# Kernel optimization log

Measured on AMD Instinct MI355X. Metric: run time of the kernel, lower is better.

Reference implementation:

```python
import jax, jax.numpy as jnp
import numpy as np

EPS = 1e-8
N_ITER = 3
S = 8      # n_slots
D = 64     # slot_size
HID = 128  # mlp hidden


def _ln(x, w, b):
    m = jnp.mean(x, axis=-1, keepdims=True)
    v = jnp.var(x, axis=-1, keepdims=True)
    return (x - m) * jax.lax.rsqrt(v + 1e-5) * w + b


def setup_inputs() -> dict:
    key = jax.random.key(0)
    ks = jax.random.split(key, 20)
    B, N, Din = 128, 4096, 64
    g = lambda k, sh, s: (jax.random.normal(k, sh, jnp.float32) * s)
    return {
        "inputs": jax.random.normal(ks[0], (B, N, Din), jnp.float32),
        "eps_noise": jax.random.normal(ks[1], (B, S, D), jnp.float32),
        "slot_mu": g(ks[2], (1, 1, D), 0.1),
        "slot_logvar": g(ks[3], (1, 1, D), 0.1),
        "k_w": g(ks[4], (D, Din), 1.0 / np.sqrt(Din)),
        "v_w": g(ks[5], (D, Din), 1.0 / np.sqrt(Din)),
        "q_w": g(ks[6], (D, D), 1.0 / np.sqrt(D)),
        "ni_w": jnp.ones((Din,), jnp.float32), "ni_b": jnp.zeros((Din,), jnp.float32),
        "ns_w": jnp.ones((D,), jnp.float32),  "ns_b": jnp.zeros((D,), jnp.float32),
        "nr_w": jnp.ones((D,), jnp.float32),  "nr_b": jnp.zeros((D,), jnp.float32),
        "gru_wih": g(ks[7], (3 * D, D), 1.0 / np.sqrt(D)),
        "gru_whh": g(ks[8], (3 * D, D), 1.0 / np.sqrt(D)),
        "gru_bih": jnp.zeros((3 * D,), jnp.float32),
        "gru_bhh": jnp.zeros((3 * D,), jnp.float32),
        "mlp_w1": g(ks[9], (HID, D), 1.0 / np.sqrt(D)),
        "mlp_w2": g(ks[10], (D, HID), 1.0 / np.sqrt(HID)),
        "mlp_b2": jnp.zeros((D,), jnp.float32),
    }


def _gru(x, h, wih, whh, bih, bhh):
    gi = x @ wih.T + bih  # [BS, 3D]
    gh = h @ whh.T + bhh
    i_r, i_z, i_n = jnp.split(gi, 3, axis=-1)
    h_r, h_z, h_n = jnp.split(gh, 3, axis=-1)
    r = jax.nn.sigmoid(i_r + h_r)
    z = jax.nn.sigmoid(i_z + h_z)
    n = jnp.tanh(i_n + r * h_n)
    return (1.0 - z) * n + z * h


def _step(slots, k, v, q_w, ns_w, ns_b, nr_w, nr_b,
          gru_wih, gru_whh, gru_bih, gru_bhh, mlp_w1, mlp_w2, mlp_b2):
    B = slots.shape[0]
    q = _ln(slots, ns_w, ns_b) @ q_w.T                     # [B,S,D]
    logits = jnp.einsum('bnd,bsd->bns', k, q)              # [B,N,S]
    w = jax.nn.softmax(logits, axis=-1) + EPS              # softmax over slots
    w = w / jnp.sum(w, axis=-2, keepdims=True)             # renorm over tokens
    atten_maps = jnp.einsum('bns,bnd->bsd', w, v)          # [B,S,D]
    h = _gru(atten_maps.reshape(B * S, D), slots.reshape(B * S, D),
             gru_wih, gru_whh, gru_bih, gru_bhh)
    h = h + (jax.nn.relu(_ln(h, nr_w, nr_b) @ mlp_w1.T) @ mlp_w2.T + mlp_b2)
    return h.reshape(B, S, D), w


def reference(inputs, eps_noise, slot_mu, slot_logvar, k_w, v_w, q_w,
              ni_w, ni_b, ns_w, ns_b, nr_w, nr_b,
              gru_wih, gru_whh, gru_bih, gru_bhh, mlp_w1, mlp_w2, mlp_b2):
    std = jnp.exp(0.5 * slot_logvar)
    slots = slot_mu + std * eps_noise                      # [B,S,D]
    x = _ln(inputs, ni_w, ni_b)
    k = (x @ k_w.T) / np.sqrt(D).astype(np.float32)        # [B,N,D]
    v = x @ v_w.T
    args = (q_w, ns_w, ns_b, nr_w, nr_b, gru_wih, gru_whh,
            gru_bih, gru_bhh, mlp_w1, mlp_w2, mlp_b2)
    for _ in range(N_ITER):
        slots, w = _step(slots, k, v, *args)
    slots, w = _step(jax.lax.stop_gradient(slots), k, v, *args)
    return slots, w
```

## Files before the change

kernel.cpp:

```cpp
#include <hip/hip_runtime.h>
#include <hip/hip_bf16.h>

#define BB 128
#define NN 4096
#define DD 64
#define SS 8
#define HH 128

typedef __attribute__((ext_vector_type(8))) short short8;
typedef __attribute__((ext_vector_type(4))) short short4v;
typedef __attribute__((ext_vector_type(4))) float f32x4;

__device__ __forceinline__ float warp_red_sum(float v) {
    #pragma unroll
    for (int off = 32; off; off >>= 1) v += __shfl_xor(v, off);
    return v;
}

__device__ __forceinline__ float bcastlane(float v, int l) {
    return __int_as_float(__builtin_amdgcn_readlane(__float_as_int(v), l));
}

__device__ __forceinline__ unsigned short bfu(float f) {
    __hip_bfloat16 h = __float2bfloat16(f);
    return *(unsigned short*)&h;
}

__device__ __forceinline__ unsigned pk2(float a, float b) {
    return (unsigned)bfu(a) | ((unsigned)bfu(b) << 16);
}

__device__ __forceinline__ short4v ds_tr16(unsigned off) {
    short4v r;
    asm volatile("ds_read_b64_tr_b16 %0, %1" : "=v"(r) : "v"(off));
    return r;
}

__global__ __launch_bounds__(256) void prep_kernel(
    const float* __restrict__ v_w, const float* __restrict__ q_w,
    const float* __restrict__ wih, const float* __restrict__ whh,
    const float* __restrict__ w1, const float* __restrict__ w2,
    float* __restrict__ vwT, float* __restrict__ qwT,
    float* __restrict__ wihT, float* __restrict__ whhT,
    float* __restrict__ w1T, float* __restrict__ w2T)
{
    int i0 = blockIdx.x * blockDim.x + threadIdx.x;
    int nthr = gridDim.x * blockDim.x;
    for (int t = i0; t < 4096; t += nthr) {
        int i = t >> 6, o = t & 63;
        vwT[t] = v_w[o * 64 + i];
        qwT[t] = q_w[o * 64 + i];
    }
    for (int t = i0; t < 12288; t += nthr) {
        int r = t / 192, c = t % 192;
        wihT[t] = wih[c * 64 + r];
        whhT[t] = whh[c * 64 + r];
    }
    for (int t = i0; t < 8192; t += nthr) {
        int r = t >> 7, c = t & 127;
        w1T[t] = w1[c * 64 + r];
    }
    for (int t = i0; t < 8192; t += nthr) {
        int r = t >> 6, c = t & 63;
        w2T[t] = w2[c * 128 + r];
    }
}

__global__ __launch_bounds__(256) void init_q_kernel(
    const float* __restrict__ eps, const float* __restrict__ mu,
    const float* __restrict__ lv, const float* __restrict__ qwT,
    const float* __restrict__ k_w,
    const float* __restrict__ nsw, const float* __restrict__ nsb,
    float* __restrict__ slots, unsigned short* __restrict__ qb,
    float* __restrict__ zbuf)
{
    const int tid = threadIdx.x, lane = tid & 63;
    const int row = blockIdx.x * 4 + (tid >> 6);
    const int idx = row * 64 + lane;
    float s0 = mu[lane] + __expf(0.5f * lv[lane]) * eps[idx];
    slots[idx] = s0;
    float m = warp_red_sum(s0) * (1.0f / 64.0f);
    float dx = s0 - m;
    float var = warp_red_sum(dx * dx) * (1.0f / 64.0f);
    float xln = dx * rsqrtf(var + 1e-5f) * nsw[lane] + nsb[lane];
    float q = 0.f;
    #pragma unroll 8
    for (int i = 0; i < 64; ++i) q = fmaf(bcastlane(xln, i), qwT[i * 64 + lane], q);
    float qp = 0.f;
    #pragma unroll 8
    for (int o = 0; o < 64; ++o) qp = fmaf(bcastlane(q, o), k_w[o * 64 + lane], qp);
    qb[idx] = bfu(qp * 0.125f);
    int g = blockIdx.x * 256 + tid;
    for (int j = g; j < 66560; j += 65536) zbuf[j] = 0.f;
}

__global__ __launch_bounds__(256) void phase_a_ln(
    const float* __restrict__ inp, const float* __restrict__ niw, const float* __restrict__ nib,
    unsigned short* __restrict__ xb)
{
    const int tid = threadIdx.x, lane = tid & 63, widx = tid >> 6;
    const int t8 = lane >> 3, d8 = lane & 7;
    const float4 wn0 = *(const float4*)&niw[d8 * 8];
    const float4 wn1 = *(const float4*)&niw[d8 * 8 + 4];
    const float4 bn0 = *(const float4*)&nib[d8 * 8];
    const float4 bn1 = *(const float4*)&nib[d8 * 8 + 4];
    const int tok0 = blockIdx.x * 128;
    #pragma unroll
    for (int it = 0; it < 4; ++it) {
        const int m = widx * 32 + it * 8 + t8;
        const float* rowp = inp + (size_t)(tok0 + m) * 64 + d8 * 8;
        float4 a = *(const float4*)rowp;
        float4 c = *(const float4*)(rowp + 4);
        float s1 = (a.x + a.y + a.z + a.w) + (c.x + c.y + c.z + c.w);
        float s2 = fmaf(a.x, a.x, fmaf(a.y, a.y, fmaf(a.z, a.z, a.w * a.w)));
        s2 = fmaf(c.x, c.x, fmaf(c.y, c.y, fmaf(c.z, c.z, fmaf(c.w, c.w, s2))));
        #pragma unroll
        for (int o = 1; o < 8; o <<= 1) { s1 += __shfl_xor(s1, o); s2 += __shfl_xor(s2, o); }
        float mean = s1 * (1.0f / 64.0f);
        float var = s2 * (1.0f / 64.0f) - mean * mean;
        float rstd = rsqrtf(var + 1e-5f);
        float y[8];
        y[0] = (a.x - mean) * rstd * wn0.x + bn0.x;
        y[1] = (a.y - mean) * rstd * wn0.y + bn0.y;
        y[2] = (a.z - mean) * rstd * wn0.z + bn0.z;
        y[3] = (a.w - mean) * rstd * wn0.w + bn0.w;
        y[4] = (c.x - mean) * rstd * wn1.x + bn1.x;
        y[5] = (c.y - mean) * rstd * wn1.y + bn1.y;
        y[6] = (c.z - mean) * rstd * wn1.z + bn1.z;
        y[7] = (c.w - mean) * rstd * wn1.w + bn1.w;
        uint4 o4;
        o4.x = pk2(y[0], y[1]); o4.y = pk2(y[2], y[3]);
        o4.z = pk2(y[4], y[5]); o4.w = pk2(y[6], y[7]);
        *(uint4*)&xb[(size_t)(tok0 + m) * 64 + d8 * 8] = o4;
    }
}

__global__ __launch_bounds__(256) void attn_mfma(
    const __hip_bfloat16* __restrict__ xb,
    const unsigned short* __restrict__ qb,
    float* __restrict__ numer, float* __restrict__ denom, float* __restrict__ wout)
{
    __shared__ unsigned short smem[11904];
    unsigned short* Qs = smem;
    const int tid = threadIdx.x, lane = tid & 63, widx = tid >> 6;
    unsigned short* wls = smem + 1152 + widx * 640;
    unsigned short* Xw  = smem + 3712 + widx * 2048;
    const int b = blockIdx.y;
    const int quad = lane >> 4, l16 = lane & 15;
    const int twave0 = blockIdx.x * 512 + widx * 128;

    short8 bkA[2][2], bkB[2][2];
    #pragma unroll
    for (int t4h = 0; t4h < 2; ++t4h) {
        const size_t xrow = ((size_t)b * NN + twave0 + t4h * 16 + l16) * 64;
        bkA[t4h][0] = *(const short8*)&xb[xrow + quad * 8];
        bkA[t4h][1] = *(const short8*)&xb[xrow + 32 + quad * 8];
    }

    for (int t = tid; t < 1024; t += 256) {
        int s = t >> 6, dd = t & 63;
        Qs[s * 72 + dd] = (s < 8) ? qb[b * 512 + t] : (unsigned short)0;
    }
    for (int t = lane; t < 320; t += 64) wls[320 + t] = 0;
    __syncthreads();

    short8 aq0 = *(const short8*)&Qs[l16 * 72 + quad * 8];
    short8 aq1 = *(const short8*)&Qs[l16 * 72 + 32 + quad * 8];

    f32x4 accv[4];
    #pragma unroll
    for (int nt = 0; nt < 4; ++nt) accv[nt] = (f32x4){0.f, 0.f, 0.f, 0.f};
    float dacc[4] = {0.f, 0.f, 0.f, 0.f};

    unsigned short* xw0 = Xw + (quad >> 1) * 512 + l16 * 16 + (quad & 1) * 8;
    const unsigned xtr = (unsigned)(size_t)Xw
                       + (unsigned)((quad * 8 + (l16 >> 2)) * 32 + (l16 & 3) * 8);

    auto PROC = [&](short8 (&cur)[2][2], short8 (&nxt)[2][2], int hg, bool pf) {
        const int t0g = twave0 + hg * 32;
        if (pf) {
            #pragma unroll
            for (int t4h = 0; t4h < 2; ++t4h) {
                const size_t xrow = ((size_t)b * NN + t0g + 32 + t4h * 16 + l16) * 64;
                nxt[t4h][0] = *(const short8*)&xb[xrow + quad * 8];
                nxt[t4h][1] = *(const short8*)&xb[xrow + 32 + quad * 8];
            }
        }
        #pragma unroll
        for (int t4h = 0; t4h < 2; ++t4h) {
            const int tok = t0g + t4h * 16 + l16;
            short8 bk0 = cur[t4h][0];
            short8 bk1 = cur[t4h][1];
            *(short8*)(xw0 + t4h * 256) = bk0;
            *(short8*)(xw0 + t4h * 256 + 1024) = bk1;
            f32x4 lg = (f32x4){0.f, 0.f, 0.f, 0.f};
            lg = __builtin_amdgcn_mfma_f32_16x16x32_bf16(aq0, bk0, lg, 0, 0, 0);
            lg = __builtin_amdgcn_mfma_f32_16x16x32_bf16(aq1, bk1, lg, 0, 0, 0);
            float e[4];
            #pragma unroll
            for (int r = 0; r < 4; ++r) e[r] = __expf(lg[r]);
            float s4 = (e[0] + e[1]) + (e[2] + e[3]);
            float stot = s4 + __shfl_xor(s4, 16);
            float rs = __builtin_amdgcn_rcpf(stot);
            float wv[4];
            #pragma unroll
            for (int r = 0; r < 4; ++r) { wv[r] = fmaf(e[r], rs, 1e-8f); dacc[r] += wv[r]; }
            if (quad < 2) {
                #pragma unroll
                for (int r = 0; r < 4; ++r)
                    wls[(quad * 4 + r) * 40 + t4h * 16 + l16] = bfu(wv[r]);
                if (wout)
                    *(float4*)&wout[((size_t)b * NN + tok) * 8 + quad * 4] =
                        make_float4(wv[0], wv[1], wv[2], wv[3]);
            }
        }
        asm volatile("" ::: "memory");
        short8 aw = *(const short8*)&wls[l16 * 40 + quad * 8];
        short4v rlo[4], rhi[4];
        #pragma unroll
        for (int nt = 0; nt < 4; ++nt) {
            rlo[nt] = ds_tr16(xtr + nt * 1024);
            rhi[nt] = ds_tr16(xtr + nt * 1024 + 128);
        }
        asm volatile("s_waitcnt lgkmcnt(0)");
        __builtin_amdgcn_sched_barrier(0);
        #pragma unroll
        for (int nt = 0; nt < 4; ++nt) {
            short8 bv = __builtin_shufflevector(rlo[nt], rhi[nt], 0, 1, 2, 3, 4, 5, 6, 7);
            accv[nt] = __builtin_amdgcn_mfma_f32_16x16x32_bf16(aw, bv, accv[nt], 0, 0, 0);
        }
    };

    PROC(bkA, bkB, 0, true);
    PROC(bkB, bkA, 1, true);
    PROC(bkA, bkB, 2, true);
    PROC(bkB, bkA, 3, false);

    #pragma unroll
    for (int r = 0; r < 4; ++r) {
        dacc[r] += __shfl_xor(dacc[r], 1);
        dacc[r] += __shfl_xor(dacc[r], 2);
        dacc[r] += __shfl_xor(dacc[r], 4);
        dacc[r] += __shfl_xor(dacc[r], 8);
    }
    __syncthreads();
    float* red = (float*)smem;
    float* dred = red + 2048;
    if (quad < 2) {
        #pragma unroll
        for (int nt = 0; nt < 4; ++nt)
            #pragma unroll
            for (int r = 0; r < 4; ++r)
                red[widx * 512 + (quad * 4 + r) * 64 + nt * 16 + l16] = accv[nt][r];
        if (l16 == 0) {
            #pragma unroll
            for (int r = 0; r < 4; ++r) dred[widx * 8 + quad * 4 + r] = dacc[r];
        }
    }
    __syncthreads();
    for (int e = tid; e < 512; e += 256)
        atomicAdd(numer + (size_t)b * 512 + e, red[e] + red[512 + e] + red[1024 + e] + red[1536 + e]);
    if (tid < 8)
        atomicAdd(denom + b * 8 + tid, dred[tid] + dred[8 + tid] + dred[16 + tid] + dred[24 + tid]);
}

__global__ __launch_bounds__(256) void gru_q_kernel(
    const float* __restrict__ numerX, const float* __restrict__ denom,
    const float* __restrict__ slotsIn,
    const float* __restrict__ vwT, const float* __restrict__ wihT, const float* __restrict__ whhT,
    const float* __restrict__ w1T, const float* __restrict__ w2T,
    const float* __restrict__ bih, const float* __restrict__ bhh,
    const float* __restrict__ nrw, const float* __restrict__ nrb,
    const float* __restrict__ b2,
    const float* __restrict__ qwT, const float* __restrict__ k_w,
    const float* __restrict__ nsw, const float* __restrict__ nsb,
    float* __restrict__ slotsOut, unsigned short* __restrict__ qb,
    float* __restrict__ zbuf)
{
    const int tid = threadIdx.x, lane = tid & 63;
    const int row = blockIdx.x * 4 + (tid >> 6);
    float nx = numerX[row * 64 + lane];
    float xp = 0.f;
    #pragma unroll 8
    for (int i = 0; i < 64; ++i) xp = fmaf(bcastlane(nx, i), vwT[i * 64 + lane], xp);
    float x = xp / denom[row];
    float h = slotsIn[row * 64 + lane];
    float air = 0, aiz = 0, ain = 0, ahr = 0, ahz = 0, ahn = 0;
    #pragma unroll 8
    for (int i = 0; i < 64; ++i) {
        float xi = bcastlane(x, i), hi = bcastlane(h, i);
        const float* wi = wihT + i * 192;
        const float* wh = whhT + i * 192;
        air = fmaf(xi, wi[lane], air);
        aiz = fmaf(xi, wi[64 + lane], aiz);
        ain = fmaf(xi, wi[128 + lane], ain);
        ahr = fmaf(hi, wh[lane], ahr);
        ahz = fmaf(hi, wh[64 + lane], ahz);
        ahn = fmaf(hi, wh[128 + lane], ahn);
    }
    air += bih[lane]; aiz += bih[64 + lane]; ain += bih[128 + lane];
    ahr += bhh[lane]; ahz += bhh[64 + lane]; ahn += bhh[128 + lane];
    float r = 1.f / (1.f + __expf(-(air + ahr)));
    float z = 1.f / (1.f + __expf(-(aiz + ahz)));
    float n = tanhf(ain + r * ahn);
    float hn = (1.f - z) * n + z * h;
    float m = warp_red_sum(hn) * (1.0f / 64.0f);
    float dx = hn - m;
    float var = warp_red_sum(dx * dx) * (1.0f / 64.0f);
    float u = dx * rsqrtf(var + 1e-5f) * nrw[lane] + nrb[lane];
    float o0 = 0.f, o1 = 0.f;
    #pragma unroll 8
    for (int i = 0; i < 64; ++i) {
        float ui = bcastlane(u, i);
        const float* w1r = w1T + i * 128;
        o0 = fmaf(ui, w1r[lane], o0);
        o1 = fmaf(ui, w1r[64 + lane], o1);
    }
    o0 = fmaxf(o0, 0.f); o1 = fmaxf(o1, 0.f);
    float y = 0.f;
    #pragma unroll 8
    for (int j = 0; j < 64; ++j) y = fmaf(bcastlane(o0, j), w2T[j * 64 + lane], y);
    #pragma unroll 8
    for (int j = 0; j < 64; ++j) y = fmaf(bcastlane(o1, j), w2T[(64 + j) * 64 + lane], y);
    y += b2[lane];
    float out = hn + y;
    slotsOut[row * 64 + lane] = out;
    float m2 = warp_red_sum(out) * (1.0f / 64.0f);
    float dx2 = out - m2;
    float var2 = warp_red_sum(dx2 * dx2) * (1.0f / 64.0f);
    float u2 = dx2 * rsqrtf(var2 + 1e-5f) * nsw[lane] + nsb[lane];
    float q = 0.f;
    #pragma unroll 8
    for (int i = 0; i < 64; ++i) q = fmaf(bcastlane(u2, i), qwT[i * 64 + lane], q);
    float qp = 0.f;
    #pragma unroll 8
    for (int o = 0; o < 64; ++o) qp = fmaf(bcastlane(q, o), k_w[o * 64 + lane], qp);
    qb[row * 64 + lane] = bfu(qp * 0.125f);
    int g = blockIdx.x * 256 + tid;
    for (int j = g; j < 66560; j += 65536) zbuf[j] = 0.f;
}

__global__ __launch_bounds__(256) void renorm_kernel(float* __restrict__ wout,
                                                     const float* __restrict__ denom)
{
    const size_t i4 = (size_t)blockIdx.x * blockDim.x + threadIdx.x;
    const size_t b = i4 >> 13;
    const int half = (int)(i4 & 1);
    float4 v = reinterpret_cast<float4*>(wout)[i4];
    const float4 dv = reinterpret_cast<const float4*>(denom)[b * 2 + half];
    v.x /= dv.x; v.y /= dv.y; v.z /= dv.z; v.w /= dv.w;
    reinterpret_cast<float4*>(wout)[i4] = v;
}

extern "C" void kernel_launch(void* const* d_in, const int* in_sizes, int n_in,
                              void* d_out, int out_size, void* d_ws, size_t ws_size,
                              hipStream_t stream)
{
    const float* inputs  = (const float*)d_in[0];
    const float* eps_n   = (const float*)d_in[1];
    const float* mu      = (const float*)d_in[2];
    const float* lv      = (const float*)d_in[3];
    const float* k_w     = (const float*)d_in[4];
    const float* v_w     = (const float*)d_in[5];
    const float* q_w     = (const float*)d_in[6];
    const float* ni_w    = (const float*)d_in[7];
    const float* ni_b    = (const float*)d_in[8];
    const float* ns_w    = (const float*)d_in[9];
    const float* ns_b    = (const float*)d_in[10];
    const float* nr_w    = (const float*)d_in[11];
    const float* nr_b    = (const float*)d_in[12];
    const float* gru_wih = (const float*)d_in[13];
    const float* gru_whh = (const float*)d_in[14];
    const float* gru_bih = (const float*)d_in[15];
    const float* gru_bhh = (const float*)d_in[16];
    const float* mlp_w1  = (const float*)d_in[17];
    const float* mlp_w2  = (const float*)d_in[18];
    const float* mlp_b2  = (const float*)d_in[19];

    char* wsb = (char*)d_ws;
    unsigned short* xb  = (unsigned short*)wsb;
    float* f      = (float*)(wsb + 134217728);
    float* slotsA = f;
    float* slotsB = f + 65536;
    unsigned short* qb = (unsigned short*)(f + 131072);
    float* numer0 = f + 163840;
    float* denom0 = f + 229376;
    float* numer1 = f + 230400;
    float* denom1 = f + 295936;
    float* vwT    = f + 296960;
    float* qwT    = f + 301056;
    float* wihT   = f + 305152;
    float* whhT   = f + 317440;
    float* w1T    = f + 329728;
    float* w2T    = f + 337920;

    float* out_slots = (float*)d_out;
    float* out_w     = out_slots + 65536;

    prep_kernel<<<64, 256, 0, stream>>>(v_w, q_w, gru_wih, gru_whh, mlp_w1, mlp_w2,
                                        vwT, qwT, wihT, whhT, w1T, w2T);
    init_q_kernel<<<256, 256, 0, stream>>>(eps_n, mu, lv, qwT, k_w, ns_w, ns_b,
                                           slotsA, qb, numer0);
    phase_a_ln<<<4096, 256, 0, stream>>>(inputs, ni_w, ni_b, xb);

    float* cur = slotsA;
    float* numers[2] = {numer0, numer1};
    float* denoms[2] = {denom0, denom1};
    for (int step = 0; step < 4; ++step) {
        int pb = step & 1;
        attn_mfma<<<dim3(8, 128), 256, 0, stream>>>((const __hip_bfloat16*)xb, qb,
                                                    numers[pb], denoms[pb],
                                                    step == 3 ? out_w : nullptr);
        float* nxt = (step == 3) ? out_slots : ((step & 1) ? slotsA : slotsB);
        gru_q_kernel<<<256, 256, 0, stream>>>(numers[pb], denoms[pb], cur,
                                              vwT, wihT, whhT, w1T, w2T,
                                              gru_bih, gru_bhh, nr_w, nr_b, mlp_b2,
                                              qwT, k_w, ns_w, ns_b,
                                              nxt, qb, numers[1 - pb]);
        cur = nxt;
    }
    renorm_kernel<<<4096, 256, 0, stream>>>(out_w, denom1);
}
```

Before: 390.3 us.

## Fuse whole slot-attention pipeline into one persistent kernel per batch

Replaces the chain of LN, init, four attention launches, four GRU launches and the renorm pass with a single kernel in which one 1024-thread block owns one batch element. Slots, queries and the numerator/denominator reductions stay in LDS, which removes global atomics, zeroing buffers and about a dozen launches. The cost is only 128 blocks on a GPU with 256 CUs, so half the machine sits idle. The per-batch GRU/MLP work is also serialised inside each block, with most waves waiting at barriers during it.

Result: slower. 757.3 us (+94.0%).

```diff
diff --git a/kernel.cpp b/kernel.cpp
--- a/kernel.cpp
+++ b/kernel.cpp
@@ -66,290 +66,280 @@
     }
 }
 
-__global__ __launch_bounds__(256) void init_q_kernel(
-    const float* __restrict__ eps, const float* __restrict__ mu,
-    const float* __restrict__ lv, const float* __restrict__ qwT,
-    const float* __restrict__ k_w,
+__global__ __launch_bounds__(1024) void batch_kernel(
+    const float* __restrict__ inp, const float* __restrict__ niw, const float* __restrict__ nib,
+    const float* __restrict__ eps, const float* __restrict__ mu, const float* __restrict__ lv,
+    const float* __restrict__ q_w, const float* __restrict__ k_w,
     const float* __restrict__ nsw, const float* __restrict__ nsb,
-    float* __restrict__ slots, unsigned short* __restrict__ qb,
-    float* __restrict__ zbuf)
+    const float* __restrict__ nrw, const float* __restrict__ nrb,
+    const float* __restrict__ bih, const float* __restrict__ bhh, const float* __restrict__ b2,
+    const float* __restrict__ vwT, const float* __restrict__ qwT,
+    const float* __restrict__ wihT, const float* __restrict__ whhT,
+    const float* __restrict__ w1T, const float* __restrict__ w2T,
+    unsigned short* __restrict__ xb,
+    float* __restrict__ out_slots, float* __restrict__ out_w)
 {
-    const int tid = threadIdx.x, lane = tid & 63;
-    const int row = blockIdx.x * 4 + (tid >> 6);
-    const int idx = row * 64 + lane;
-    float s0 = mu[lane] + __expf(0.5f * lv[lane]) * eps[idx];
-    slots[idx] = s0;
-    float m = warp_red_sum(s0) * (1.0f / 64.0f);
-    float dx = s0 - m;
-    float var = warp_red_sum(dx * dx) * (1.0f / 64.0f);
-    float xln = dx * rsqrtf(var + 1e-5f) * nsw[lane] + nsb[lane];
-    float q = 0.f;
-    #pragma unroll 8
-    for (int i = 0; i < 64; ++i) q = fmaf(bcastlane(xln, i), qwT[i * 64 + lane], q);
-    float qp = 0.f;
-    #pragma unroll 8
-    for (int o = 0; o < 64; ++o) qp = fmaf(bcastlane(q, o), k_w[o * 64 + lane], qp);
-    qb[idx] = bfu(qp * 0.125f);
-    int g = blockIdx.x * 256 + tid;
-    for (int j = g; j < 66560; j += 65536) zbuf[j] = 0.f;
-}
-
-__global__ __launch_bounds__(256) void phase_a_ln(
-    const float* __restrict__ inp, const float* __restrict__ niw, const float* __restrict__ nib,
-    unsigned short* __restrict__ xb)
-{
+    __shared__ unsigned short smem[61184];
+    __shared__ float denom_lds[8];
+    const int b = blockIdx.x;
     const int tid = threadIdx.x, lane = tid & 63, widx = tid >> 6;
-    const int t8 = lane >> 3, d8 = lane & 7;
-    const float4 wn0 = *(const float4*)&niw[d8 * 8];
-    const float4 wn1 = *(const float4*)&niw[d8 * 8 + 4];
-    const float4 bn0 = *(const float4*)&nib[d8 * 8];
-    const float4 bn1 = *(const float4*)&nib[d8 * 8 + 4];
-    const int tok0 = blockIdx.x * 128;
-    #pragma unroll
-    for (int it = 0; it < 4; ++it) {
-        const int m = widx * 32 + it * 8 + t8;
-        const float* rowp = inp + (size_t)(tok0 + m) * 64 + d8 * 8;
-        float4 a = *(const float4*)rowp;
-        float4 c = *(const float4*)(rowp + 4);
-        float s1 = (a.x + a.y + a.z + a.w) + (c.x + c.y + c.z + c.w);
-        float s2 = fmaf(a.x, a.x, fmaf(a.y, a.y, fmaf(a.z, a.z, a.w * a.w)));
-        s2 = fmaf(c.x, c.x, fmaf(c.y, c.y, fmaf(c.z, c.z, fmaf(c.w, c.w, s2))));
-        #pragma unroll
-        for (int o = 1; o < 8; o <<= 1) { s1 += __shfl_xor(s1, o); s2 += __shfl_xor(s2, o); }
-        float mean = s1 * (1.0f / 64.0f);
-        float var = s2 * (1.0f / 64.0f) - mean * mean;
-        float rstd = rsqrtf(var + 1e-5f);
-        float y[8];
-        y[0] = (a.x - mean) * rstd * wn0.x + bn0.x;
-        y[1] = (a.y - mean) * rstd * wn0.y + bn0.y;
-        y[2] = (a.z - mean) * rstd * wn0.z + bn0.z;
-        y[3] = (a.w - mean) * rstd * wn0.w + bn0.w;
-        y[4] = (c.x - mean) * rstd * wn1.x + bn1.x;
-        y[5] = (c.y - mean) * rstd * wn1.y + bn1.y;
-        y[6] = (c.z - mean) * rstd * wn1.z + bn1.z;
-        y[7] = (c.w - mean) * rstd * wn1.w + bn1.w;
-        uint4 o4;
-        o4.x = pk2(y[0], y[1]); o4.y = pk2(y[2], y[3]);
-        o4.z = pk2(y[4], y[5]); o4.w = pk2(y[6], y[7]);
-        *(uint4*)&xb[(size_t)(tok0 + m) * 64 + d8 * 8] = o4;
-    }
-}
-
-__global__ __launch_bounds__(256) void attn_mfma(
-    const __hip_bfloat16* __restrict__ xb,
-    const unsigned short* __restrict__ qb,
-    float* __restrict__ numer, float* __restrict__ denom, float* __restrict__ wout)
-{
-    __shared__ unsigned short smem[11904];
-    unsigned short* Qs = smem;
-    const int tid = threadIdx.x, lane = tid & 63, widx = tid >> 6;
-    unsigned short* wls = smem + 1152 + widx * 640;
-    unsigned short* Xw  = smem + 3712 + widx * 2048;
-    const int b = blockIdx.y;
     const int quad = lane >> 4, l16 = lane & 15;
-    const int twave0 = blockIdx.x * 512 + widx * 128;
-
-    short8 bkA[2][2], bkB[2][2];
-    #pragma unroll
-    for (int t4h = 0; t4h < 2; ++t4h) {
-        const size_t xrow = ((size_t)b * NN + twave0 + t4h * 16 + l16) * 64;
-        bkA[t4h][0] = *(const short8*)&xb[xrow + quad * 8];
-        bkA[t4h][1] = *(const short8*)&xb[xrow + 32 + quad * 8];
-    }
-
-    for (int t = tid; t < 1024; t += 256) {
-        int s = t >> 6, dd = t & 63;
-        Qs[s * 72 + dd] = (s < 8) ? qb[b * 512 + t] : (unsigned short)0;
+    unsigned short* wls = smem + widx * 640;
+    unsigned short* Xw  = smem + 10240 + widx * 2048;
+    float* red  = (float*)(smem + 43008);
+    float* dred = (float*)(smem + 59392);
+    unsigned short* qb_lds = smem + 59648;
+    float* slots_lds = (float*)(smem + 60160);
+
+    {
+        const int t8 = lane >> 3, d8 = lane & 7;
+        const float4 wn0 = *(const float4*)&niw[d8 * 8];
+        const float4 wn1 = *(const float4*)&niw[d8 * 8 + 4];
+        const float4 bn0 = *(const float4*)&nib[d8 * 8];
+        const float4 bn1 = *(const float4*)&nib[d8 * 8 + 4];
+        #pragma unroll 4
+        for (int it = 0; it < 32; ++it) {
+            const int m = widx * 256 + it * 8 + t8;
+            const float* rowp = inp + ((size_t)b * NN + m) * 64 + d8 * 8;
+            float4 a = *(const float4*)rowp;
+            float4 c = *(const float4*)(rowp + 4);
+            float s1 = (a.x + a.y + a.z + a.w) + (c.x + c.y + c.z + c.w);
+            float s2 = fmaf(a.x, a.x, fmaf(a.y, a.y, fmaf(a.z, a.z, a.w * a.w)));
+            s2 = fmaf(c.x, c.x, fmaf(c.y, c.y, fmaf(c.z, c.z, fmaf(c.w, c.w, s2))));
+            #pragma unroll
+            for (int o = 1; o < 8; o <<= 1) { s1 += __shfl_xor(s1, o); s2 += __shfl_xor(s2, o); }
+            float mean = s1 * (1.0f / 64.0f);
+            float var = s2 * (1.0f / 64.0f) - mean * mean;
+            float rstd = rsqrtf(var + 1e-5f);
+            float y[8];
+            y[0] = (a.x - mean) * rstd * wn0.x + bn0.x;
+            y[1] = (a.y - mean) * rstd * wn0.y + bn0.y;
+            y[2] = (a.z - mean) * rstd * wn0.z + bn0.z;
+            y[3] = (a.w - mean) * rstd * wn0.w + bn0.w;
+            y[4] = (c.x - mean) * rstd * wn1.x + bn1.x;
+            y[5] = (c.y - mean) * rstd * wn1.y + bn1.y;
+            y[6] = (c.z - mean) * rstd * wn1.z + bn1.z;
+            y[7] = (c.w - mean) * rstd * wn1.w + bn1.w;
+            uint4 o4;
+            o4.x = pk2(y[0], y[1]); o4.y = pk2(y[2], y[3]);
+            o4.z = pk2(y[4], y[5]); o4.w = pk2(y[6], y[7]);
+            *(uint4*)&xb[((size_t)b * NN + m) * 64 + d8 * 8] = o4;
+        }
+    }
+    if (widx < 8) {
+        const int ss = widx;
+        const int idx = (b * 8 + ss) * 64 + lane;
+        float s0 = mu[lane] + __expf(0.5f * lv[lane]) * eps[idx];
+        slots_lds[ss * 64 + lane] = s0;
+        float m = warp_red_sum(s0) * (1.0f / 64.0f);
+        float dx = s0 - m;
+        float var = warp_red_sum(dx * dx) * (1.0f / 64.0f);
+        float xln = dx * rsqrtf(var + 1e-5f) * nsw[lane] + nsb[lane];
+        float q = 0.f;
+        #pragma unroll 8
+        for (int i = 0; i < 64; ++i) q = fmaf(bcastlane(xln, i), q_w[lane * 64 + i], q);
+        float qp = 0.f;
+        #pragma unroll 8
+        for (int o = 0; o < 64; ++o) qp = fmaf(bcastlane(q, o), k_w[o * 64 + lane], qp);
+        qb_lds[ss * 64 + lane] = bfu(qp * 0.125f);
     }
     for (int t = lane; t < 320; t += 64) wls[320 + t] = 0;
     __syncthreads();
-
-    short8 aq0 = *(const short8*)&Qs[l16 * 72 + quad * 8];
-    short8 aq1 = *(const short8*)&Qs[l16 * 72 + 32 + quad * 8];
-
-    f32x4 accv[4];
-    #pragma unroll
-    for (int nt = 0; nt < 4; ++nt) accv[nt] = (f32x4){0.f, 0.f, 0.f, 0.f};
-    float dacc[4] = {0.f, 0.f, 0.f, 0.f};
 
     unsigned short* xw0 = Xw + (quad >> 1) * 512 + l16 * 16 + (quad & 1) * 8;
     const unsigned xtr = (unsigned)(size_t)Xw
                        + (unsigned)((quad * 8 + (l16 >> 2)) * 32 + (l16 & 3) * 8);
-
-    auto PROC = [&](short8 (&cur)[2][2], short8 (&nxt)[2][2], int hg, bool pf) {
-        const int t0g = twave0 + hg * 32;
-        if (pf) {
+    const int twave0 = widx * 256;
+
+    for (int s = 0; s < 4; ++s) {
+        const bool last = (s == 3);
+        short8 aq0 = (short8){0, 0, 0, 0, 0, 0, 0, 0};
+        short8 aq1 = (short8){0, 0, 0, 0, 0, 0, 0, 0};
+        if (l16 < 8) {
+            aq0 = *(const short8*)&qb_lds[l16 * 64 + quad * 8];
+            aq1 = *(const short8*)&qb_lds[l16 * 64 + 32 + quad * 8];
+        }
+        f32x4 accv[4];
+        #pragma unroll
+        for (int nt = 0; nt < 4; ++nt) accv[nt] = (f32x4){0.f, 0.f, 0.f, 0.f};
+        float dacc[4] = {0.f, 0.f, 0.f, 0.f};
+
+        short8 bkA[2][2], bkB[2][2];
+        #pragma unroll
+        for (int t4h = 0; t4h < 2; ++t4h) {
+            const size_t xrow = ((size_t)b * NN + twave0 + t4h * 16 + l16) * 64;
+            bkA[t4h][0] = *(const short8*)&xb[xrow + quad * 8];
+            bkA[t4h][1] = *(const short8*)&xb[xrow + 32 + quad * 8];
+        }
+
+        auto PROC = [&](short8 (&cur)[2][2], short8 (&nxt)[2][2], int hg, bool pf) {
+            const int t0g = twave0 + hg * 32;
+            if (pf) {
+                #pragma unroll
+                for (int t4h = 0; t4h < 2; ++t4h) {
+                    const size_t xrow = ((size_t)b * NN + t0g + 32 + t4h * 16 + l16) * 64;
+                    nxt[t4h][0] = *(const short8*)&xb[xrow + quad * 8];
+                    nxt[t4h][1] = *(const short8*)&xb[xrow + 32 + quad * 8];
+                }
+            }
             #pragma unroll
             for (int t4h = 0; t4h < 2; ++t4h) {
-                const size_t xrow = ((size_t)b * NN + t0g + 32 + t4h * 16 + l16) * 64;
-                nxt[t4h][0] = *(const short8*)&xb[xrow + quad * 8];
-                nxt[t4h][1] = *(const short8*)&xb[xrow + 32 + quad * 8];
-            }
-        }
-        #pragma unroll
-        for (int t4h = 0; t4h < 2; ++t4h) {
-            const int tok = t0g + t4h * 16 + l16;
-            short8 bk0 = cur[t4h][0];
-            short8 bk1 = cur[t4h][1];
-            *(short8*)(xw0 + t4h * 256) = bk0;
-            *(short8*)(xw0 + t4h * 256 + 1024) = bk1;
-            f32x4 lg = (f32x4){0.f, 0.f, 0.f, 0.f};
-            lg = __builtin_amdgcn_mfma_f32_16x16x32_bf16(aq0, bk0, lg, 0, 0, 0);
-            lg = __builtin_amdgcn_mfma_f32_16x16x32_bf16(aq1, bk1, lg, 0, 0, 0);
-            float e[4];
-            #pragma unroll
-            for (int r = 0; r < 4; ++r) e[r] = __expf(lg[r]);
-            float s4 = (e[0] + e[1]) + (e[2] + e[3]);
-            float stot = s4 + __shfl_xor(s4, 16);
-            float rs = __builtin_amdgcn_rcpf(stot);
-            float wv[4];
-            #pragma unroll
-            for (int r = 0; r < 4; ++r) { wv[r] = fmaf(e[r], rs, 1e-8f); dacc[r] += wv[r]; }
-            if (quad < 2) {
+                const int tok = t0g + t4h * 16 + l16;
+                short8 bk0 = cur[t4h][0];
+                short8 bk1 = cur[t4h][1];
+                *(short8*)(xw0 + t4h * 256) = bk0;
+                *(short8*)(xw0 + t4h * 256 + 1024) = bk1;
+                f32x4 lg = (f32x4){0.f, 0.f, 0.f, 0.f};
+                lg = __builtin_amdgcn_mfma_f32_16x16x32_bf16(aq0, bk0, lg, 0, 0, 0);
+                lg = __builtin_amdgcn_mfma_f32_16x16x32_bf16(aq1, bk1, lg, 0, 0, 0);
+                float e[4];
+                #pragma unroll
+                for (int r = 0; r < 4; ++r) e[r] = __expf(lg[r]);
+                float s4 = (e[0] + e[1]) + (e[2] + e[3]);
+                float stot = s4 + __shfl_xor(s4, 16);
+                float rs = __builtin_amdgcn_rcpf(stot);
+                float wv[4];
+                #pragma unroll
+                for (int r = 0; r < 4; ++r) { wv[r] = fmaf(e[r], rs, 1e-8f); dacc[r] += wv[r]; }
+                if (quad < 2) {
+                    #pragma unroll
+                    for (int r = 0; r < 4; ++r)
+                        wls[(quad * 4 + r) * 40 + t4h * 16 + l16] = bfu(wv[r]);
+                    if (last)
+                        *(float4*)&out_w[((size_t)b * NN + tok) * 8 + quad * 4] =
+                            make_float4(wv[0], wv[1], wv[2], wv[3]);
+                }
+            }
+            asm volatile("" ::: "memory");
+            short8 aw = *(const short8*)&wls[l16 * 40 + quad * 8];
+            short4v rlo[4], rhi[4];
+            #pragma unroll
+            for (int nt = 0; nt < 4; ++nt) {
+                rlo[nt] = ds_tr16(xtr + nt * 1024);
+                rhi[nt] = ds_tr16(xtr + nt * 1024 + 128);
+            }
+            asm volatile("s_waitcnt lgkmcnt(0)");
+            __builtin_amdgcn_sched_barrier(0);
+            #pragma unroll
+            for (int nt = 0; nt < 4; ++nt) {
+                short8 bv = __builtin_shufflevector(rlo[nt], rhi[nt], 0, 1, 2, 3, 4, 5, 6, 7);
+                accv[nt] = __builtin_amdgcn_mfma_f32_16x16x32_bf16(aw, bv, accv[nt], 0, 0, 0);
+            }
+        };
+
+        #pragma unroll
+        for (int hg = 0; hg < 8; ++hg) {
+            if ((hg & 1) == 0) PROC(bkA, bkB, hg, hg < 7);
+            else               PROC(bkB, bkA, hg, hg < 7);
+        }
+
+        #pragma unroll
+        for (int r = 0; r < 4; ++r) {
+            dacc[r] += __shfl_xor(dacc[r], 1);
+            dacc[r] += __shfl_xor(dacc[r], 2);
+            dacc[r] += __shfl_xor(dacc[r], 4);
+            dacc[r] += __shfl_xor(dacc[r], 8);
+        }
+        if (quad < 2) {
+            #pragma unroll
+            for (int nt = 0; nt < 4; ++nt)
                 #pragma unroll
                 for (int r = 0; r < 4; ++r)
-                    wls[(quad * 4 + r) * 40 + t4h * 16 + l16] = bfu(wv[r]);
-                if (wout)
-                    *(float4*)&wout[((size_t)b * NN + tok) * 8 + quad * 4] =
-                        make_float4(wv[0], wv[1], wv[2], wv[3]);
-            }
-        }
-        asm volatile("" ::: "memory");
-        short8 aw = *(const short8*)&wls[l16 * 40 + quad * 8];
-        short4v rlo[4], rhi[4];
-        #pragma unroll
-        for (int nt = 0; nt < 4; ++nt) {
-            rlo[nt] = ds_tr16(xtr + nt * 1024);
-            rhi[nt] = ds_tr16(xtr + nt * 1024 + 128);
-        }
-        asm volatile("s_waitcnt lgkmcnt(0)");
-        __builtin_amdgcn_sched_barrier(0);
-        #pragma unroll
-        for (int nt = 0; nt < 4; ++nt) {
-            short8 bv = __builtin_shufflevector(rlo[nt], rhi[nt], 0, 1, 2, 3, 4, 5, 6, 7);
-            accv[nt] = __builtin_amdgcn_mfma_f32_16x16x32_bf16(aw, bv, accv[nt], 0, 0, 0);
-        }
-    };
-
-    PROC(bkA, bkB, 0, true);
-    PROC(bkB, bkA, 1, true);
-    PROC(bkA, bkB, 2, true);
-    PROC(bkB, bkA, 3, false);
-
-    #pragma unroll
-    for (int r = 0; r < 4; ++r) {
-        dacc[r] += __shfl_xor(dacc[r], 1);
-        dacc[r] += __shfl_xor(dacc[r], 2);
-        dacc[r] += __shfl_xor(dacc[r], 4);
-        dacc[r] += __shfl_xor(dacc[r], 8);
-    }
-    __syncthreads();
-    float* red = (float*)smem;
-    float* dred = red + 2048;
-    if (quad < 2) {
-        #pragma unroll
-        for (int nt = 0; nt < 4; ++nt)
-            #pragma unroll
-            for (int r = 0; r < 4; ++r)
-                red[widx * 512 + (quad * 4 + r) * 64 + nt * 16 + l16] = accv[nt][r];
-        if (l16 == 0) {
-            #pragma unroll
-            for (int r = 0; r < 4; ++r) dred[widx * 8 + quad * 4 + r] = dacc[r];
-        }
-    }
-    __syncthreads();
-    for (int e = tid; e < 512; e += 256)
-        atomicAdd(numer + (size_t)b * 512 + e, red[e] + red[512 + e] + red[1024 + e] + red[1536 + e]);
-    if (tid < 8)
-        atomicAdd(denom + b * 8 + tid, dred[tid] + dred[8 + tid] + dred[16 + tid] + dred[24 + tid]);
-}
-
-__global__ __launch_bounds__(256) void gru_q_kernel(
-    const float* __restrict__ numerX, const float* __restrict__ denom,
-    const float* __restrict__ slotsIn,
-    const float* __restrict__ vwT, const float* __restrict__ wihT, const float* __restrict__ whhT,
-    const float* __restrict__ w1T, const float* __restrict__ w2T,
-    const float* __restrict__ bih, const float* __restrict__ bhh,
-    const float* __restrict__ nrw, const float* __restrict__ nrb,
-    const float* __restrict__ b2,
-    const float* __restrict__ qwT, const float* __restrict__ k_w,
-    const float* __restrict__ nsw, const float* __restrict__ nsb,
-    float* __restrict__ slotsOut, unsigned short* __restrict__ qb,
-    float* __restrict__ zbuf)
-{
-    const int tid = threadIdx.x, lane = tid & 63;
-    const int row = blockIdx.x * 4 + (tid >> 6);
-    float nx = numerX[row * 64 + lane];
-    float xp = 0.f;
-    #pragma unroll 8
-    for (int i = 0; i < 64; ++i) xp = fmaf(bcastlane(nx, i), vwT[i * 64 + lane], xp);
-    float x = xp / denom[row];
-    float h = slotsIn[row * 64 + lane];
-    float air = 0, aiz = 0, ain = 0, ahr = 0, ahz = 0, ahn = 0;
-    #pragma unroll 8
-    for (int i = 0; i < 64; ++i) {
-        float xi = bcastlane(x, i), hi = bcastlane(h, i);
-        const float* wi = wihT + i * 192;
-        const float* wh = whhT + i * 192;
-        air = fmaf(xi, wi[lane], air);
-        aiz = fmaf(xi, wi[64 + lane], aiz);
-        ain = fmaf(xi, wi[128 + lane], ain);
-        ahr = fmaf(hi, wh[lane], ahr);
-        ahz = fmaf(hi, wh[64 + lane], ahz);
-        ahn = fmaf(hi, wh[128 + lane], ahn);
-    }
-    air += bih[lane]; aiz += bih[64 + lane]; ain += bih[128 + lane];
-    ahr += bhh[lane]; ahz += bhh[64 + lane]; ahn += bhh[128 + lane];
-    float r = 1.f / (1.f + __expf(-(air + ahr)));
-    float z = 1.f / (1.f + __expf(-(aiz + ahz)));
-    float n = tanhf(ain + r * ahn);
-    float hn = (1.f - z) * n + z * h;
-    float m = warp_red_sum(hn) * (1.0f / 64.0f);
-    float dx = hn - m;
-    float var = warp_red_sum(dx * dx) * (1.0f / 64.0f);
-    float u = dx * rsqrtf(var + 1e-5f) * nrw[lane] + nrb[lane];
-    float o0 = 0.f, o1 = 0.f;
-    #pragma unroll 8
-    for (int i = 0; i < 64; ++i) {
-        float ui = bcastlane(u, i);
-        const float* w1r = w1T + i * 128;
-        o0 = fmaf(ui, w1r[lane], o0);
-        o1 = fmaf(ui, w1r[64 + lane], o1);
-    }
-    o0 = fmaxf(o0, 0.f); o1 = fmaxf(o1, 0.f);
-    float y = 0.f;
-    #pragma unroll 8
-    for (int j = 0; j < 64; ++j) y = fmaf(bcastlane(o0, j), w2T[j * 64 + lane], y);
-    #pragma unroll 8
-    for (int j = 0; j < 64; ++j) y = fmaf(bcastlane(o1, j), w2T[(64 + j) * 64 + lane], y);
-    y += b2[lane];
-    float out = hn + y;
-    slotsOut[row * 64 + lane] = out;
-    float m2 = warp_red_sum(out) * (1.0f / 64.0f);
-    float dx2 = out - m2;
-    float var2 = warp_red_sum(dx2 * dx2) * (1.0f / 64.0f);
-    float u2 = dx2 * rsqrtf(var2 + 1e-5f) * nsw[lane] + nsb[lane];
-    float q = 0.f;
-    #pragma unroll 8
-    for (int i = 0; i < 64; ++i) q = fmaf(bcastlane(u2, i), qwT[i * 64 + lane], q);
-    float qp = 0.f;
-    #pragma unroll 8
-    for (int o = 0; o < 64; ++o) qp = fmaf(bcastlane(q, o), k_w[o * 64 + lane], qp);
-    qb[row * 64 + lane] = bfu(qp * 0.125f);
-    int g = blockIdx.x * 256 + tid;
-    for (int j = g; j < 66560; j += 65536) zbuf[j] = 0.f;
-}
-
-__global__ __launch_bounds__(256) void renorm_kernel(float* __restrict__ wout,
-                                                     const float* __restrict__ denom)
-{
-    const size_t i4 = (size_t)blockIdx.x * blockDim.x + threadIdx.x;
-    const size_t b = i4 >> 13;
-    const int half = (int)(i4 & 1);
-    float4 v = reinterpret_cast<float4*>(wout)[i4];
-    const float4 dv = reinterpret_cast<const float4*>(denom)[b * 2 + half];
-    v.x /= dv.x; v.y /= dv.y; v.z /= dv.z; v.w /= dv.w;
-    reinterpret_cast<float4*>(wout)[i4] = v;
+                    red[widx * 512 + (quad * 4 + r) * 64 + nt * 16 + l16] = accv[nt][r];
+            if (l16 == 0) {
+                #pragma unroll
+                for (int r = 0; r < 4; ++r) dred[widx * 8 + quad * 4 + r] = dacc[r];
+            }
+        }
+        __syncthreads();
+
+        if (widx < 8) {
+            const int ss = widx;
+            float nx = 0.f, dt = 0.f;
+            #pragma unroll
+            for (int w = 0; w < 16; ++w) {
+                nx += red[w * 512 + ss * 64 + lane];
+                dt += dred[w * 8 + ss];
+            }
+            float xp = 0.f;
+            #pragma unroll 8
+            for (int i = 0; i < 64; ++i) xp = fmaf(bcastlane(nx, i), vwT[i * 64 + lane], xp);
+            float x = xp / dt;
+            float h = slots_lds[ss * 64 + lane];
+            float air = 0, aiz = 0, ain = 0, ahr = 0, ahz = 0, ahn = 0;
+            #pragma unroll 8
+            for (int i = 0; i < 64; ++i) {
+                float xi = bcastlane(x, i), hi = bcastlane(h, i);
+                const float* wi = wihT + i * 192;
+                const float* wh = whhT + i * 192;
+                air = fmaf(xi, wi[lane], air);
+                aiz = fmaf(xi, wi[64 + lane], aiz);
+                ain = fmaf(xi, wi[128 + lane], ain);
+                ahr = fmaf(hi, wh[lane], ahr);
+                ahz = fmaf(hi, wh[64 + lane], ahz);
+                ahn = fmaf(hi, wh[128 + lane], ahn);
+            }
+            air += bih[lane]; aiz += bih[64 + lane]; ain += bih[128 + lane];
+            ahr += bhh[lane]; ahz += bhh[64 + lane]; ahn += bhh[128 + lane];
+            float r = 1.f / (1.f + __expf(-(air + ahr)));
+            float z = 1.f / (1.f + __expf(-(aiz + ahz)));
+            float n = tanhf(ain + r * ahn);
+            float hn = (1.f - z) * n + z * h;
+            float m = warp_red_sum(hn) * (1.0f / 64.0f);
+            float dx = hn - m;
+            float var = warp_red_sum(dx * dx) * (1.0f / 64.0f);
+            float u = dx * rsqrtf(var + 1e-5f) * nrw[lane] + nrb[lane];
+            float o0 = 0.f, o1 = 0.f;
+            #pragma unroll 8
+            for (int i = 0; i < 64; ++i) {
+                float ui = bcastlane(u, i);
+                const float* w1r = w1T + i * 128;
+                o0 = fmaf(ui, w1r[lane], o0);
+                o1 = fmaf(ui, w1r[64 + lane], o1);
+            }
+            o0 = fmaxf(o0, 0.f); o1 = fmaxf(o1, 0.f);
+            float y = 0.f;
+            #pragma unroll 8
+            for (int j = 0; j < 64; ++j) y = fmaf(bcastlane(o0, j), w2T[j * 64 + lane], y);
+            #pragma unroll 8
+            for (int j = 0; j < 64; ++j) y = fmaf(bcastlane(o1, j), w2T[(64 + j) * 64 + lane], y);
+            y += b2[lane];
+            float out = hn + y;
+            if (last) {
+                out_slots[((size_t)b * 8 + ss) * 64 + lane] = out;
+                if (lane == 0) denom_lds[ss] = dt;
+            } else {
+                slots_lds[ss * 64 + lane] = out;
+                float m2 = warp_red_sum(out) * (1.0f / 64.0f);
+                float dx2 = out - m2;
+                float var2 = warp_red_sum(dx2 * dx2) * (1.0f / 64.0f);
+                float u2 = dx2 * rsqrtf(var2 + 1e-5f) * nsw[lane] + nsb[lane];
+                float q = 0.f;
+                #pragma unroll 8
+                for (int i = 0; i < 64; ++i) q = fmaf(bcastlane(u2, i), qwT[i * 64 + lane], q);
+                float qp = 0.f;
+                #pragma unroll 8
+                for (int o = 0; o < 64; ++o) qp = fmaf(bcastlane(q, o), k_w[o * 64 + lane], qp);
+                qb_lds[ss * 64 + lane] = bfu(qp * 0.125f);
+            }
+        }
+        __syncthreads();
+    }
+
+    {
+        float4* w4 = (float4*)(out_w + (size_t)b * NN * 8);
+        #pragma unroll
+        for (int it = 0; it < 8; ++it) {
+            const int idx = it * 1024 + tid;
+            const int half = idx & 1;
+            float4 v = w4[idx];
+            v.x /= denom_lds[half * 4 + 0];
+            v.y /= denom_lds[half * 4 + 1];
+            v.z /= denom_lds[half * 4 + 2];
+            v.w /= denom_lds[half * 4 + 3];
+            w4[idx] = v;
+        }
+    }
 }
 
 extern "C" void kernel_launch(void* const* d_in, const int* in_sizes, int n_in,
@@ -380,13 +370,6 @@
     char* wsb = (char*)d_ws;
     unsigned short* xb  = (unsigned short*)wsb;
     float* f      = (float*)(wsb + 134217728);
-    float* slotsA = f;
-    float* slotsB = f + 65536;
-    unsigned short* qb = (unsigned short*)(f + 131072);
-    float* numer0 = f + 163840;
-    float* denom0 = f + 229376;
-    float* numer1 = f + 230400;
-    float* denom1 = f + 295936;
     float* vwT    = f + 296960;
     float* qwT    = f + 301056;
     float* wihT   = f + 305152;
@@ -399,25 +382,9 @@
 
     prep_kernel<<<64, 256, 0, stream>>>(v_w, q_w, gru_wih, gru_whh, mlp_w1, mlp_w2,
                                         vwT, qwT, wihT, whhT, w1T, w2T);
-    init_q_kernel<<<256, 256, 0, stream>>>(eps_n, mu, lv, qwT, k_w, ns_w, ns_b,
-                                           slotsA, qb, numer0);
-    phase_a_ln<<<4096, 256, 0, stream>>>(inputs, ni_w, ni_b, xb);
-
-    float* cur = slotsA;
-    float* numers[2] = {numer0, numer1};
-    float* denoms[2] = {denom0, denom1};
-    for (int step = 0; step < 4; ++step) {
-        int pb = step & 1;
-        attn_mfma<<<dim3(8, 128), 256, 0, stream>>>((const __hip_bfloat16*)xb, qb,
-                                                    numers[pb], denoms[pb],
-                                                    step == 3 ? out_w : nullptr);
-        float* nxt = (step == 3) ? out_slots : ((step & 1) ? slotsA : slotsB);
-        gru_q_kernel<<<256, 256, 0, stream>>>(numers[pb], denoms[pb], cur,
-                                              vwT, wihT, whhT, w1T, w2T,
-                                              gru_bih, gru_bhh, nr_w, nr_b, mlp_b2,
-                                              qwT, k_w, ns_w, ns_b,
-                                              nxt, qb, numers[1 - pb]);
-        cur = nxt;
-    }
-    renorm_kernel<<<4096, 256, 0, stream>>>(out_w, denom1);
-}
+    batch_kernel<<<128, 1024, 0, stream>>>(inputs, ni_w, ni_b, eps_n, mu, lv,
+                                           q_w, k_w, ns_w, ns_b, nr_w, nr_b,
+                                           gru_bih, gru_bhh, mlp_b2,
+                                           vwT, qwT, wihT, whhT, w1T, w2T,
+                                           xb, out_slots, out_w);
+}
```
